# Performance work log

Measured on AMD Instinct MI355X. Metric: run time of the kernel, lower is better.

Reference implementation:

```python
import jax, jax.numpy as jnp
import numpy as np

B, C, M, NH, F_, W = 2, 8, 8, 8, 1024, 512  # batch, channels, attention_maps, heads, features, frames
HD = F_ // NH
EXP = 4


def _conv(x, w, b):
    y = jax.lax.conv_general_dilated(x, w, (1, 1), 'SAME',
                                     dimension_numbers=('NCHW', 'OIHW', 'NCHW'))
    return y + b[None, :, None, None]


def _rope(x):
    # x: (..., seq, d); lucidrains-style interleaved rotary embedding
    d, n = x.shape[-1], x.shape[-2]
    inv = 1.0 / (10000.0 ** (jnp.arange(0, d, 2, dtype=jnp.float32) / d))
    fr = jnp.repeat(jnp.arange(n, dtype=jnp.float32)[:, None] * inv[None, :], 2, axis=-1)
    cos, sin = jnp.cos(fr), jnp.sin(fr)
    xr = jnp.stack((-x[..., 1::2], x[..., 0::2]), axis=-1).reshape(x.shape)
    return x * cos + xr * sin


def _mcln(x, w, b, eps=1e-5):
    # MultichannelLayerNorm: normalize over features axis (axis=2 of B,C,F,W)
    mu = jnp.mean(x, axis=2, keepdims=True)
    var = jnp.var(x, axis=2, keepdims=True)
    return (x - mu) / jnp.sqrt(var + eps) * w[None, :, :, None] + b[None, :, :, None]


def _mclin(x, w_pw):
    # MultichannelLinear positionwise: per-channel matmul over features
    return jnp.einsum('bcfw,cgf->bcgw', x, w_pw)


def setup_inputs() -> dict:
    key = jax.random.key(0)
    ks = jax.random.split(key, 24)
    s = 0.02
    d = {
        'x': jax.random.normal(ks[0], (B, C, F_, W), jnp.float32),
        'prev_qk': jax.random.normal(ks[1], (B, M, NH, W, W), jnp.float32),
        'qconv_w': jax.random.normal(ks[2], (M, C, 3, 3), jnp.float32) * s,
        'qconv_b': jnp.zeros((M,), jnp.float32),
        'q_pw': jax.random.normal(ks[3], (M, F_, F_), jnp.float32) * s,
        'kconv_w': jax.random.normal(ks[4], (M, C, 3, 3), jnp.float32) * s,
        'kconv_b': jnp.zeros((M,), jnp.float32),
        'k_pw': jax.random.normal(ks[5], (M, F_, F_), jnp.float32) * s,
        'vconv_w': jax.random.normal(ks[6], (M, C, 3, 3), jnp.float32) * s,
        'vconv_b': jnp.zeros((M,), jnp.float32),
        'v_pw': jax.random.normal(ks[7], (M, F_, F_), jnp.float32) * s,
        'o_pw': jax.random.normal(ks[8], (M, F_, F_), jnp.float32) * s,
        'o_dw': jax.random.normal(ks[9], (M, M), jnp.float32) * s,
        'oproj_w': jax.random.normal(ks[10], (C, C + M, 3, 3), jnp.float32) * s,
        'oproj_b': jnp.zeros((C,), jnp.float32),
        'n1_w': jnp.ones((C, F_), jnp.float32),
        'n1_b': jnp.zeros((C, F_), jnp.float32),
        'c1_w': jax.random.normal(ks[11], (C * EXP, C, 3, 3), jnp.float32) * s,
        'c1_b': jnp.zeros((C * EXP,), jnp.float32),
        'c2_w': jax.random.normal(ks[12], (C, C * EXP, 3, 3), jnp.float32) * s,
        'c2_b': jnp.zeros((C,), jnp.float32),
        'n2_w': jnp.ones((C, F_), jnp.float32),
        'n2_b': jnp.zeros((C, F_), jnp.float32),
    }
    return d


def _encoder(x, prev_qk, qconv_w, qconv_b, q_pw, kconv_w, kconv_b, k_pw,
             vconv_w, vconv_b, v_pw, o_pw, o_dw, oproj_w, oproj_b,
             n1_w, n1_b, c1_w, c1_b, c2_w, c2_b, n2_w, n2_b):
    b, c, h, w = x.shape

    def heads(y):  # (B,M,F,W) -> (B,M,NH,W,HD)
        return y.transpose(0, 1, 3, 2).reshape(b, M, w, NH, HD).transpose(0, 1, 3, 2, 4)

    q = _rope(heads(_mclin(_conv(x, qconv_w, qconv_b), q_pw)))
    k = _rope(heads(_mclin(_conv(x, kconv_w, kconv_b), k_pw)))
    v = heads(_mclin(_conv(x, vconv_w, vconv_b), v_pw))

    qk = jnp.einsum('bmnqd,bmnkd->bmnqk', q, k) / jnp.sqrt(jnp.float32(h))
    qk = qk + prev_qk
    a = jnp.einsum('bmnqk,bmnkd->bmnqd', jax.nn.softmax(qk, axis=-1), v)
    a = a.transpose(0, 1, 3, 2, 4).reshape(b, M, w, NH * HD).transpose(0, 1, 3, 2)  # (B,M,F,W)
    a = jnp.einsum('bcfw,dc->bdfw', _mclin(a, o_pw), o_dw)  # depthwise o_linear
    z = _conv(jnp.concatenate((x, a), axis=1), oproj_w, oproj_b)

    hid = _mcln(x + z, n1_w, n1_b)  # dropout is identity in eval
    z2 = _conv(jax.nn.gelu(_conv(hid, c1_w, c1_b), approximate=False), c2_w, c2_b)
    out = _mcln(hid + z2, n2_w, n2_b)
    return out, qk


def reference(x, prev_qk, qconv_w, qconv_b, q_pw, kconv_w, kconv_b, k_pw,
              vconv_w, vconv_b, v_pw, o_pw, o_dw, oproj_w, oproj_b,
              n1_w, n1_b, c1_w, c1_b, c2_w, c2_b, n2_w, n2_b):
    out, qk = _encoder(x, prev_qk, qconv_w, qconv_b, q_pw, kconv_w, kconv_b, k_pw,
                       vconv_w, vconv_b, v_pw, o_pw, o_dw, oproj_w, oproj_b,
                       n1_w, n1_b, c1_w, c1_b, c2_w, c2_b, n2_w, n2_b)
    return (out, out, qk)
```

## Files before the change

### kernel.cpp

```cpp
#include <hip/hip_runtime.h>
#include <math.h>

#define B_ 2
#define C_ 8
#define M_ 8
#define NH_ 8
#define F_ 1024
#define W_ 512
#define HD_ 128
#define FW 524288L
#define PF_ 1026
#define PW_ 514

typedef __bf16 bf16_t;
typedef __bf16 bf16x8 __attribute__((ext_vector_type(8)));
typedef __bf16 bf16x4 __attribute__((ext_vector_type(4)));
typedef float f32x4 __attribute__((ext_vector_type(4)));

__device__ __forceinline__ void gload16(const void* g, void* l) {
    __builtin_amdgcn_global_load_lds(
        (const __attribute__((address_space(1))) unsigned int*)g,
        (__attribute__((address_space(3))) unsigned int*)l,
        16, 0, 0);
}

__device__ __forceinline__ float gelu_f(float v) {
    return 0.5f * v * (1.0f + erff(v * 0.70710678118f));
}

__global__ __launch_bounds__(256)
void pad_stage_k(const float* __restrict__ x, bf16_t* __restrict__ px)
{
    long i = (long)blockIdx.x * 256 + threadIdx.x;
    if (i >= (long)B_ * PF_ * PW_) return;
    int wc = (int)(i % PW_);
    long t = i / PW_;
    int fr = (int)(t % PF_);
    int b  = (int)(t / PF_);
    bf16x8 v = {};
    if (fr >= 1 && fr <= F_ && wc >= 1 && wc <= W_) {
        const float* s = x + (long)b * 8 * FW + (long)(fr - 1) * W_ + (wc - 1);
        #pragma unroll
        for (int c = 0; c < 8; ++c) v[c] = (bf16_t)s[c * FW];
    }
    *(bf16x8*)&px[i * 8] = v;
}

__global__ __launch_bounds__(256)
void borderz8_k(bf16_t* __restrict__ p8a, bf16_t* __restrict__ p8b)
{
    int i = blockIdx.x * 256 + threadIdx.x;
    if (i >= 2 * 3076) return;
    int b = i / 3076, p = i % 3076;
    int fr, wc;
    if (p < 514)       { fr = 0;    wc = p; }
    else if (p < 1028) { fr = 1025; wc = p - 514; }
    else if (p < 2052) { fr = 1 + (p - 1028); wc = 0; }
    else               { fr = 1 + (p - 2052); wc = 513; }
    long pix = ((long)b * PF_ + fr) * PW_ + wc;
    bf16x8 z = {};
    *(bf16x8*)&p8a[pix * 8] = z;
    *(bf16x8*)&p8b[pix * 8] = z;
}

__global__ __launch_bounds__(256)
void borderz32_k(bf16_t* __restrict__ p32)
{
    int i = blockIdx.x * 256 + threadIdx.x;
    if (i >= 2 * 3076) return;
    int b = i / 3076, p = i % 3076;
    int fr, wc;
    if (p < 514)       { fr = 0;    wc = p; }
    else if (p < 1028) { fr = 1025; wc = p - 514; }
    else if (p < 2052) { fr = 1 + (p - 1028); wc = 0; }
    else               { fr = 1 + (p - 2052); wc = 513; }
    long pix = ((long)b * PF_ + fr) * PW_ + wc;
    bf16x8 z = {};
    #pragma unroll
    for (int k = 0; k < 4; ++k) *(bf16x8*)&p32[pix * 32 + k * 8] = z;
}

__global__ void aprep_k(const float* __restrict__ qw, const float* __restrict__ kw,
                        const float* __restrict__ vw, const float* __restrict__ ow,
                        const float* __restrict__ c1w, const float* __restrict__ c2w,
                        const float* __restrict__ qb, const float* __restrict__ kb,
                        const float* __restrict__ vb,
                        bf16_t* __restrict__ a_qkv, bf16_t* __restrict__ a_op,
                        bf16_t* __restrict__ a_c1, bf16_t* __restrict__ a_c2,
                        float* __restrict__ bias_qkv)
{
    int mode = blockIdx.y;
    int i = blockIdx.x * 256 + threadIdx.x;
    if (mode == 0) {
        if (i < 3072) {
            int k = i & 31, co = (i >> 5) & 31, df = i >> 10;
            int tap = k >> 3, ci = k & 7;
            float v = 0.f;
            if (tap < 3) {
                if (co < 8)       v = qw[((co * 8 + ci) * 3 + df) * 3 + tap];
                else if (co < 16) v = kw[(((co - 8) * 8 + ci) * 3 + df) * 3 + tap];
                else if (co < 24) v = vw[(((co - 16) * 8 + ci) * 3 + df) * 3 + tap];
            }
            a_qkv[i] = (bf16_t)v;
        }
        if (i < 32) bias_qkv[i] = (i < 8) ? qb[i] : (i < 16) ? kb[i - 8] : (i < 24) ? vb[i - 16] : 0.f;
    } else if (mode == 1) {
        if (i < 3072) {
            int k = i & 63, co = (i >> 6) & 15, df = i >> 10;
            int src = k >> 5, r = k & 31, tap = r >> 3, ci = src * 8 + (r & 7);
            float v = 0.f;
            if (co < 8 && tap < 3) v = ow[((co * 16 + ci) * 3 + df) * 3 + tap];
            a_op[i] = (bf16_t)v;
        }
    } else if (mode == 2) {
        if (i < 3072) {
            int k = i & 31, co = (i >> 5) & 31, df = i >> 10;
            int tap = k >> 3, ci = k & 7;
            float v = (tap < 3) ? c1w[((co * 8 + ci) * 3 + df) * 3 + tap] : 0.f;
            a_c1[i] = (bf16_t)v;
        }
    } else {
        if (i < 4608) {
            int k = i % 96, co = (i / 96) & 15, df = i / (96 * 16);
            int tap = k >> 5, ci = k & 31;
            float v = (co < 8) ? c2w[((co * 32 + ci) * 3 + df) * 3 + tap] : 0.f;
            a_c2[i] = (bf16_t)v;
        }
    }
}

template<int CIN, int KSTEPS, int MFRAGS, int DUAL, int EPI>
__global__ __launch_bounds__(256)
void convg_k(const bf16_t* __restrict__ px0, const bf16_t* __restrict__ px1,
             const bf16_t* __restrict__ Ab, const float* __restrict__ bias,
             const float* __restrict__ resid, void* __restrict__ outp)
{
    const int f = blockIdx.y, b = blockIdx.z;
    const int tid = threadIdx.x, lane = tid & 63, wid = tid >> 6;
    const int l15 = lane & 15, l4 = lane >> 4;
    const int wbase = blockIdx.x * 256 + wid * 64;
    const int KW = KSTEPS * 32, M16 = MFRAGS * 16;

    bf16x8 af[3][MFRAGS][KSTEPS];
    #pragma unroll
    for (int df = 0; df < 3; ++df)
        #pragma unroll
        for (int mf = 0; mf < MFRAGS; ++mf)
            #pragma unroll
            for (int kk = 0; kk < KSTEPS; ++kk)
                af[df][mf][kk] = *(const bf16x8*)&Ab[(long)(df * M16 + mf * 16 + l15) * KW + kk * 32 + l4 * 8];

    f32x4 acc[MFRAGS][4];
    #pragma unroll
    for (int mf = 0; mf < MFRAGS; ++mf)
        #pragma unroll
        for (int nf = 0; nf < 4; ++nf)
            acc[mf][nf] = (f32x4){0.f, 0.f, 0.f, 0.f};

    #pragma unroll
    for (int df = 0; df < 3; ++df) {
        const long rowb = ((long)(b * PF_ + f + df)) * PW_ * CIN;
        #pragma unroll
        for (int nf = 0; nf < 4; ++nf) {
            const int wp = wbase + nf * 16 + l15;
            #pragma unroll
            for (int kk = 0; kk < KSTEPS; ++kk) {
                const bf16_t* src = (DUAL && kk == 1) ? px1 : px0;
                long addr = (CIN == 8) ? rowb + (long)(wp + l4) * 8
                                       : rowb + (long)(wp + kk) * 32 + l4 * 8;
                bf16x8 bv = *(const bf16x8*)&src[addr];
                #pragma unroll
                for (int mf = 0; mf < MFRAGS; ++mf)
                    acc[mf][nf] = __builtin_amdgcn_mfma_f32_16x16x32_bf16(
                        af[df][mf][kk], bv, acc[mf][nf], 0, 0, 0);
            }
        }
    }

    #pragma unroll
    for (int mf = 0; mf < MFRAGS; ++mf) {
        #pragma unroll
        for (int nf = 0; nf < 4; ++nf) {
            const int wp = wbase + nf * 16 + l15;
            if (EPI == 2) {
                const int cob = mf * 16 + l4 * 4;
                bf16x4 ov;
                #pragma unroll
                for (int r = 0; r < 4; ++r)
                    ov[r] = (bf16_t)gelu_f(acc[mf][nf][r] + bias[cob + r]);
                *(bf16x4*)&((bf16_t*)outp)[(((long)(b * PF_ + f + 1)) * PW_ + wp + 1) * 32 + cob] = ov;
            } else {
                #pragma unroll
                for (int r = 0; r < 4; ++r) {
                    const int co = mf * 16 + l4 * 4 + r;
                    float v = acc[mf][nf][r];
                    if (EPI == 0) {
                        if (co < 24)
                            ((bf16_t*)outp)[((long)(b * 24 + co)) * FW + (long)f * W_ + wp] = (bf16_t)(v + bias[co]);
                    } else {
                        if (co < 8) {
                            long oi = ((long)(b * 8 + co)) * FW + (long)f * W_ + wp;
                            ((bf16_t*)outp)[oi] = (bf16_t)(v + bias[co] + resid[oi]);
                        }
                    }
                }
            }
        }
    }
}

template<int EPI, int OUTBF>
__global__ __launch_bounds__(256)
void gemm_mfma_k(const bf16_t* __restrict__ Ab, const bf16_t* __restrict__ Bb,
                 void* __restrict__ Cb, const float* __restrict__ Addb,
                 float scale, int Kdim, int lda, int ldb, int ldc,
                 long sA, long sB, long sC_hi, long sC_lo, int zdivC,
                 long sAdd, int aMod)
{
    __shared__ bf16_t sAt[4096];
    __shared__ bf16_t sBt[4096];

    const int z = blockIdx.z;
    const bf16_t* A = Ab + (long)(z % aMod) * sA;
    const bf16_t* B = Bb + (long)z * sB;
    const int m0 = blockIdx.y * 128;
    const int n0 = blockIdx.x * 128;
    const int tid = threadIdx.x;
    const int lane = tid & 63, wid = tid >> 6;
    const int wr = (wid >> 1) * 64, wc = (wid & 1) * 64;
    const int l15 = lane & 15, l4 = lane >> 4;

    f32x4 acc[4][4];
    #pragma unroll
    for (int m = 0; m < 4; ++m)
        #pragma unroll
        for (int n = 0; n < 4; ++n)
            acc[m][n] = (f32x4){0.f, 0.f, 0.f, 0.f};

    const int srow = tid >> 2;
    const int scol = (tid & 3) * 8;
    const long gA0 = (long)(m0 + srow) * lda + scol;
    const long gA1 = (long)(m0 + 64 + srow) * lda + scol;
    const long gB0 = (long)(n0 + srow) * ldb + scol;
    const long gB1 = (long)(n0 + 64 + srow) * ldb + scol;
    bf16_t* lA = sAt + wid * 512;
    bf16_t* lB = sBt + wid * 512;

    for (int k0 = 0; k0 < Kdim; k0 += 32) {
        __syncthreads();
        gload16(A + gA0 + k0, lA);
        gload16(A + gA1 + k0, lA + 2048);
        gload16(B + gB0 + k0, lB);
        gload16(B + gB1 + k0, lB + 2048);
        __syncthreads();

        bf16x8 afr[4], bfr[4];
        #pragma unroll
        for (int m = 0; m < 4; ++m)
            afr[m] = *(const bf16x8*)&sAt[(wr + m * 16 + l15) * 32 + l4 * 8];
        #pragma unroll
        for (int n = 0; n < 4; ++n)
            bfr[n] = *(const bf16x8*)&sBt[(wc + n * 16 + l15) * 32 + l4 * 8];
        #pragma unroll
        for (int m = 0; m < 4; ++m)
            #pragma unroll
            for (int n = 0; n < 4; ++n)
                acc[m][n] = __builtin_amdgcn_mfma_f32_16x16x32_bf16(
                    afr[m], bfr[n], acc[m][n], 0, 0, 0);
    }

    if (EPI == 2) {
        #pragma unroll
        for (int m = 0; m < 4; ++m) {
            const int d0 = wr + m * 16 + l4 * 4;
            const float inv0 = __expf(-(float)(d0 >> 1) * 0.14391156507f);
            const float inv1 = __expf(-(float)((d0 >> 1) + 1) * 0.14391156507f);
            #pragma unroll
            for (int n = 0; n < 4; ++n) {
                const int col = n0 + wc + n * 16 + l15;
                float s0, c0, s1, c1;
                __sincosf((float)col * inv0, &s0, &c0);
                __sincosf((float)col * inv1, &s1, &c1);
                float v0 = acc[m][n][0], v1 = acc[m][n][1];
                float v2 = acc[m][n][2], v3 = acc[m][n][3];
                bf16x4 ov = { (bf16_t)(v0 * c0 - v1 * s0), (bf16_t)(v1 * c0 + v0 * s0),
                              (bf16_t)(v2 * c1 - v3 * s1), (bf16_t)(v3 * c1 + v2 * s1) };
                *(bf16x4*)&((bf16_t*)Cb)[(((long)z * 8 + blockIdx.y) * 512 + col) * 128 + d0] = ov;
            }
        }
        return;
    }

    const long zc = (long)(z / zdivC) * sC_hi + (long)(z % zdivC) * sC_lo;
    #pragma unroll
    for (int m = 0; m < 4; ++m) {
        #pragma unroll
        for (int n = 0; n < 4; ++n) {
            #pragma unroll
            for (int r = 0; r < 4; ++r) {
                int row = m0 + wr + m * 16 + l4 * 4 + r;
                int col = n0 + wc + n * 16 + l15;
                float v = acc[m][n][r];
                if (EPI == 1) v = v * scale + Addb[(long)z * sAdd + (long)row * ldc + col];
                long cidx = zc + (long)row * ldc + col;
                if (OUTBF) ((bf16_t*)Cb)[cidx] = (bf16_t)v;
                else       ((float*)Cb)[cidx]  = v;
            }
        }
    }
}

__global__ __launch_bounds__(256)
void tcvt_k(const bf16_t* __restrict__ in, bf16_t* __restrict__ outp, int smul, int sbase)
{
    __shared__ float tile[32][33];
    const int w0 = blockIdx.x * 32, f0 = blockIdx.y * 32;
    const int z = blockIdx.z;
    const int inSlice = (z >> 3) * smul + sbase + (z & 7);
    const long ibase = (long)inSlice * FW;
    const long obase = (long)z * FW;
    const int tx = threadIdx.x & 31, ty = threadIdx.x >> 5;
    #pragma unroll
    for (int i = 0; i < 4; ++i)
        tile[ty + i * 8][tx] = (float)in[ibase + (long)(f0 + ty + i * 8) * W_ + w0 + tx];
    __syncthreads();
    #pragma unroll
    for (int i = 0; i < 4; ++i)
        outp[obase + (long)(w0 + ty + i * 8) * F_ + f0 + tx] = (bf16_t)tile[tx][ty + i * 8];
}

__global__ __launch_bounds__(256)
void cvt_k(const float* __restrict__ in, bf16_t* __restrict__ o, int n4)
{
    int i = blockIdx.x * 256 + threadIdx.x;
    if (i < n4) {
        float4 v = ((const float4*)in)[i];
        bf16x4 r = { (bf16_t)v.x, (bf16_t)v.y, (bf16_t)v.z, (bf16_t)v.w };
        *(bf16x4*)&o[(long)i * 4] = r;
    }
}

__device__ inline float waveMax(float v) {
    #pragma unroll
    for (int o = 32; o >= 1; o >>= 1) v = fmaxf(v, __shfl_xor(v, o, 64));
    return v;
}
__device__ inline float waveSum(float v) {
    #pragma unroll
    for (int o = 32; o >= 1; o >>= 1) v += __shfl_xor(v, o, 64);
    return v;
}

__global__ __launch_bounds__(256)
void softmax_k(const float* __restrict__ S, bf16_t* __restrict__ P)
{
    const int wid = threadIdx.x >> 6, lane = threadIdx.x & 63;
    const long row = (long)blockIdx.x * 4 + wid;
    const float4* s4 = (const float4*)(S + row * 512);
    float4 a = s4[lane * 2], b = s4[lane * 2 + 1];
    float m = fmaxf(fmaxf(fmaxf(a.x, a.y), fmaxf(a.z, a.w)),
                    fmaxf(fmaxf(b.x, b.y), fmaxf(b.z, b.w)));
    m = waveMax(m);
    float e0 = __expf(a.x - m), e1 = __expf(a.y - m), e2 = __expf(a.z - m), e3 = __expf(a.w - m);
    float e4 = __expf(b.x - m), e5 = __expf(b.y - m), e6 = __expf(b.z - m), e7 = __expf(b.w - m);
    float su = waveSum(e0 + e1 + e2 + e3 + e4 + e5 + e6 + e7);
    float inv = 1.0f / su;
    bf16x8 o = { (bf16_t)(e0 * inv), (bf16_t)(e1 * inv), (bf16_t)(e2 * inv), (bf16_t)(e3 * inv),
                 (bf16_t)(e4 * inv), (bf16_t)(e5 * inv), (bf16_t)(e6 * inv), (bf16_t)(e7 * inv) };
    *(bf16x8*)(P + row * 512 + lane * 8) = o;
}

__global__ __launch_bounds__(256)
void odw_k(const bf16_t* __restrict__ t, const float* __restrict__ dw, bf16_t* __restrict__ px)
{
    long i = (long)blockIdx.x * 256 + threadIdx.x;
    int w = (int)(i & (W_ - 1));
    long q = i >> 9;
    int f = (int)(q & (F_ - 1));
    int b = (int)(q >> 10);
    const bf16_t* s = t + (long)b * 8 * FW + (long)f * W_ + w;
    float tv[8];
    #pragma unroll
    for (int c = 0; c < 8; ++c) tv[c] = (float)s[c * FW];
    bf16x8 o;
    #pragma unroll
    for (int d = 0; d < 8; ++d) {
        float a = 0.f;
        #pragma unroll
        for (int c = 0; c < 8; ++c) a += tv[c] * dw[d * 8 + c];
        o[d] = (bf16_t)a;
    }
    *(bf16x8*)&px[(((long)b * PF_ + f + 1) * PW_ + w + 1) * 8] = o;
}

template<typename TIN>
__global__ __launch_bounds__(256)
void mcln_k(const TIN* __restrict__ in, const float* __restrict__ gam,
            const float* __restrict__ bet, float* __restrict__ o1, float* __restrict__ o2,
            bf16_t* __restrict__ px)
{
    int wi = threadIdx.x & 31, fg = threadIdx.x >> 5;
    int w0 = blockIdx.x * 32;
    int c = blockIdx.y, b = blockIdx.z;
    long base = ((long)b * C_ + c) * FW + w0 + wi;
    float s = 0.f, q = 0.f;
    for (int f = fg; f < F_; f += 8) {
        float v = (float)in[base + (long)f * W_];
        s += v; q += v * v;
    }
    __shared__ float rs[8][33], rq[8][33];
    __shared__ float mu_s[32], inv_s[32];
    rs[fg][wi] = s; rq[fg][wi] = q;
    __syncthreads();
    if (fg == 0) {
        float ts = 0.f, tq = 0.f;
        for (int g = 0; g < 8; ++g) { ts += rs[g][wi]; tq += rq[g][wi]; }
        float mu = ts * (1.0f / F_);
        float var = tq * (1.0f / F_) - mu * mu;
        mu_s[wi] = mu;
        inv_s[wi] = rsqrtf(var + 1e-5f);
    }
    __syncthreads();
    float mu = mu_s[wi], inv = inv_s[wi];
    for (int f = fg; f < F_; f += 8) {
        float v = (float)in[base + (long)f * W_];
        float r = (v - mu) * inv * gam[c * F_ + f] + bet[c * F_ + f];
        long oi = base + (long)f * W_;
        o1[oi] = r;
        if (o2) o2[oi] = r;
        if (px) px[(((long)b * PF_ + f + 1) * PW_ + (w0 + wi) + 1) * 8 + c] = (bf16_t)r;
    }
}

extern "C" void kernel_launch(void* const* d_in, const int* in_sizes, int n_in,
                              void* d_out, int out_size, void* d_ws, size_t ws_size,
                              hipStream_t stream) {
    (void)in_sizes; (void)n_in; (void)out_size; (void)ws_size;
    const float* x        = (const float*)d_in[0];
    const float* prev_qk  = (const float*)d_in[1];
    const float* qconv_w  = (const float*)d_in[2];
    const float* qconv_b  = (const float*)d_in[3];
    const float* q_pw     = (const float*)d_in[4];
    const float* kconv_w  = (const float*)d_in[5];
    const float* kconv_b  = (const float*)d_in[6];
    const float* k_pw     = (const float*)d_in[7];
    const float* vconv_w  = (const float*)d_in[8];
    const float* vconv_b  = (const float*)d_in[9];
    const float* v_pw     = (const float*)d_in[10];
    const float* o_pw     = (const float*)d_in[11];
    const float* o_dw     = (const float*)d_in[12];
    const float* oproj_w  = (const float*)d_in[13];
    const float* oproj_b  = (const float*)d_in[14];
    const float* n1_w     = (const float*)d_in[15];
    const float* n1_b     = (const float*)d_in[16];
    const float* c1_w     = (const float*)d_in[17];
    const float* c1_b     = (const float*)d_in[18];
    const float* c2_w     = (const float*)d_in[19];
    const float* c2_b     = (const float*)d_in[20];
    const float* n2_w     = (const float*)d_in[21];
    const float* n2_b     = (const float*)d_in[22];

    float* out    = (float*)d_out;
    float* qk_out = out + 16777216L;

    char* wsb = (char*)d_ws;
    bf16_t* PX8  = (bf16_t*)(wsb + 0L);
    bf16_t* Wq   = (bf16_t*)(wsb + 16876032L);
    bf16_t* Wk   = (bf16_t*)(wsb + 33653248L);
    bf16_t* Wv   = (bf16_t*)(wsb + 50430464L);
    bf16_t* Wo   = (bf16_t*)(wsb + 67207680L);
    bf16_t* QR   = (bf16_t*)(wsb + 83984896L);
    bf16_t* KR   = (bf16_t*)(wsb + 100762112L);
    bf16_t* VL   = (bf16_t*)(wsb + 117539328L);
    bf16_t* QKV  = (bf16_t*)(wsb + 134316544L);
    bf16_t* XT   = (bf16_t*)(wsb + 184648192L);
    bf16_t* SH   = (bf16_t*)(wsb + 134316544L);
    bf16_t* AT   = (bf16_t*)(wsb + 201425408L);
    bf16_t* F1b  = (bf16_t*)(wsb + 83984896L);
    bf16_t* PXA2 = (bf16_t*)(wsb + 100762112L);
    bf16_t* PRE  = (bf16_t*)(wsb + 134316544L);
    float*  HID  = (float*) (wsb + 151093760L);
    bf16_t* PXH  = (bf16_t*)(wsb + 218202624L);
    bf16_t* PXC1 = (bf16_t*)(wsb + 0L);
    bf16_t* ABQ  = (bf16_t*)(wsb + 235078400L);
    bf16_t* ABO  = (bf16_t*)(wsb + 235078400L + 16384L);
    bf16_t* ABC1 = (bf16_t*)(wsb + 235078400L + 32768L);
    bf16_t* ABC2 = (bf16_t*)(wsb + 235078400L + 49152L);
    float*  BQKV = (float*) (wsb + 235078400L + 65536L);

    const dim3 cvgrid(2, F_, B_);
    const dim3 tgrid(16, 32, 16);
    const dim3 ggrid(4, 8, 16);
    const long BIG = 1 << 30;

    cvt_k<<<8192, 256, 0, stream>>>(q_pw, Wq, 2097152);
    cvt_k<<<8192, 256, 0, stream>>>(k_pw, Wk, 2097152);
    cvt_k<<<8192, 256, 0, stream>>>(v_pw, Wv, 2097152);
    cvt_k<<<8192, 256, 0, stream>>>(o_pw, Wo, 2097152);
    aprep_k<<<dim3(18, 4), 256, 0, stream>>>(qconv_w, kconv_w, vconv_w, oproj_w, c1_w, c2_w,
                                             qconv_b, kconv_b, vconv_b,
                                             ABQ, ABO, ABC1, ABC2, BQKV);
    pad_stage_k<<<4121, 256, 0, stream>>>(x, PX8);

    convg_k<8, 1, 2, 0, 0><<<cvgrid, 256, 0, stream>>>(PX8, nullptr, ABQ, BQKV, nullptr, QKV);

    tcvt_k<<<tgrid, 256, 0, stream>>>(QKV, XT, 24, 0);
    gemm_mfma_k<2, 1><<<ggrid, 256, 0, stream>>>(Wq, XT, QR, nullptr, 1.f,
        F_, F_, F_, W_, 1048576L, 524288L, 0L, 0L, 1, 0L, 8);

    tcvt_k<<<tgrid, 256, 0, stream>>>(QKV, XT, 24, 8);
    gemm_mfma_k<2, 1><<<ggrid, 256, 0, stream>>>(Wk, XT, KR, nullptr, 1.f,
        F_, F_, F_, W_, 1048576L, 524288L, 0L, 0L, 1, 0L, 8);

    tcvt_k<<<tgrid, 256, 0, stream>>>(QKV, XT, 24, 16);
    gemm_mfma_k<0, 1><<<ggrid, 256, 0, stream>>>(Wv, XT, VL, nullptr, 1.f,
        F_, F_, F_, W_, 1048576L, 524288L, 524288L, 0L, 1, 0L, 8);

    gemm_mfma_k<1, 0><<<dim3(4, 4, 128), 256, 0, stream>>>(QR, KR, qk_out, prev_qk,
        0.03125f, HD_, HD_, HD_, W_, 65536L, 65536L, 262144L, 0L, 1, 262144L, (int)BIG);
    softmax_k<<<16384, 256, 0, stream>>>(qk_out, SH);
    gemm_mfma_k<0, 1><<<dim3(1, 4, 128), 256, 0, stream>>>(SH, VL, AT, nullptr, 1.f,
        W_, W_, W_, F_, 262144L, 65536L, 524288L, 128L, 8, 0L, (int)BIG);

    gemm_mfma_k<0, 1><<<ggrid, 256, 0, stream>>>(Wo, AT, F1b, nullptr, 1.f,
        F_, F_, F_, W_, 1048576L, 524288L, 524288L, 0L, 1, 0L, 8);
    odw_k<<<4096, 256, 0, stream>>>(F1b, o_dw, PXA2);
    borderz8_k<<<25, 256, 0, stream>>>(PXA2, PXH);

    convg_k<8, 2, 1, 1, 1><<<cvgrid, 256, 0, stream>>>(PX8, PXA2, ABO, oproj_b, x, PRE);
    borderz32_k<<<25, 256, 0, stream>>>(PXC1);

    mcln_k<bf16_t><<<dim3(16, 8, 2), 256, 0, stream>>>(PRE, n1_w, n1_b, HID, nullptr, PXH);

    convg_k<8, 1, 2, 0, 2><<<cvgrid, 256, 0, stream>>>(PXH, nullptr, ABC1, c1_b, nullptr, PXC1);
    convg_k<32, 3, 1, 0, 1><<<cvgrid, 256, 0, stream>>>(PXC1, nullptr, ABC2, c2_b, HID, PRE);
    mcln_k<bf16_t><<<dim3(16, 8, 2), 256, 0, stream>>>(PRE, n2_w, n2_b, out, out + 8388608L, nullptr);
}
```

Baseline: 705.8 us.

## Fuse fp32 weight conversion into GEMM loads, widen K tile, batch transposes

```diff
diff --git a/kernel.cpp b/kernel.cpp
--- a/kernel.cpp
+++ b/kernel.cpp
@@ -209,20 +209,18 @@
     }
 }
 
-template<int EPI, int OUTBF>
-__global__ __launch_bounds__(256)
-void gemm_mfma_k(const bf16_t* __restrict__ Ab, const bf16_t* __restrict__ Bb,
+template<int EPI, int OUTBF, int AF32>
+__global__ __launch_bounds__(256)
+void gemm_mfma_k(const void* __restrict__ Ab_, const bf16_t* __restrict__ Bb,
                  void* __restrict__ Cb, const float* __restrict__ Addb,
                  float scale, int Kdim, int lda, int ldb, int ldc,
                  long sA, long sB, long sC_hi, long sC_lo, int zdivC,
                  long sAdd, int aMod)
 {
-    __shared__ bf16_t sAt[4096];
-    __shared__ bf16_t sBt[4096];
+    __shared__ bf16_t sAt[8192];
+    __shared__ bf16_t sBt[8192];
 
     const int z = blockIdx.z;
-    const bf16_t* A = Ab + (long)(z % aMod) * sA;
-    const bf16_t* B = Bb + (long)z * sB;
     const int m0 = blockIdx.y * 128;
     const int n0 = blockIdx.x * 128;
     const int tid = threadIdx.x;
@@ -230,6 +228,10 @@
     const int wr = (wid >> 1) * 64, wc = (wid & 1) * 64;
     const int l15 = lane & 15, l4 = lane >> 4;
 
+    const bf16_t* A16 = AF32 ? nullptr : (const bf16_t*)Ab_ + (long)(z % aMod) * sA;
+    const float*  A32 = AF32 ? (const float*)Ab_ + (long)(z % aMod) * sA : nullptr;
+    const bf16_t* B = Bb + (long)z * sB;
+
     f32x4 acc[4][4];
     #pragma unroll
     for (int m = 0; m < 4; ++m)
@@ -237,36 +239,61 @@
         for (int n = 0; n < 4; ++n)
             acc[m][n] = (f32x4){0.f, 0.f, 0.f, 0.f};
 
-    const int srow = tid >> 2;
-    const int scol = (tid & 3) * 8;
-    const long gA0 = (long)(m0 + srow) * lda + scol;
-    const long gA1 = (long)(m0 + 64 + srow) * lda + scol;
-    const long gB0 = (long)(n0 + srow) * ldb + scol;
-    const long gB1 = (long)(n0 + 64 + srow) * ldb + scol;
-    bf16_t* lA = sAt + wid * 512;
-    bf16_t* lB = sBt + wid * 512;
-
-    for (int k0 = 0; k0 < Kdim; k0 += 32) {
+    const int grow = wid * 8 + (lane >> 3);
+    const int gslot = lane & 7;
+    const int arow = tid >> 1;
+    const int akg  = (tid & 1) * 4;
+
+    for (int k0 = 0; k0 < Kdim; k0 += 64) {
         __syncthreads();
-        gload16(A + gA0 + k0, lA);
-        gload16(A + gA1 + k0, lA + 2048);
-        gload16(B + gB0 + k0, lB);
-        gload16(B + gB1 + k0, lB + 2048);
+        if (AF32) {
+            const float* asrc = A32 + (long)(m0 + arow) * lda + k0 + akg * 8;
+            const int swz = arow & 7;
+            #pragma unroll
+            for (int j = 0; j < 4; ++j) {
+                float4 u = ((const float4*)asrc)[j * 2];
+                float4 v = ((const float4*)asrc)[j * 2 + 1];
+                bf16x8 w8 = { (bf16_t)u.x, (bf16_t)u.y, (bf16_t)u.z, (bf16_t)u.w,
+                              (bf16_t)v.x, (bf16_t)v.y, (bf16_t)v.z, (bf16_t)v.w };
+                *(bf16x8*)&sAt[arow * 64 + (((akg + j) ^ swz) << 3)] = w8;
+            }
+        } else {
+            #pragma unroll
+            for (int r = 0; r < 4; ++r) {
+                const int row = r * 32 + grow;
+                gload16(A16 + (long)(m0 + row) * lda + k0 + ((gslot ^ (row & 7)) << 3),
+                        sAt + r * 2048 + wid * 512);
+            }
+        }
+        #pragma unroll
+        for (int r = 0; r < 4; ++r) {
+            const int row = r * 32 + grow;
+            gload16(B + (long)(n0 + row) * ldb + k0 + ((gslot ^ (row & 7)) << 3),
+                    sBt + r * 2048 + wid * 512);
+        }
         __syncthreads();
 
-        bf16x8 afr[4], bfr[4];
-        #pragma unroll
-        for (int m = 0; m < 4; ++m)
-            afr[m] = *(const bf16x8*)&sAt[(wr + m * 16 + l15) * 32 + l4 * 8];
-        #pragma unroll
-        for (int n = 0; n < 4; ++n)
-            bfr[n] = *(const bf16x8*)&sBt[(wc + n * 16 + l15) * 32 + l4 * 8];
-        #pragma unroll
-        for (int m = 0; m < 4; ++m)
-            #pragma unroll
-            for (int n = 0; n < 4; ++n)
-                acc[m][n] = __builtin_amdgcn_mfma_f32_16x16x32_bf16(
-                    afr[m], bfr[n], acc[m][n], 0, 0, 0);
+        bf16x8 afr[4][2], bfr[4][2];
+        #pragma unroll
+        for (int m = 0; m < 4; ++m) {
+            const int row = wr + m * 16 + l15, swz = row & 7;
+            afr[m][0] = *(const bf16x8*)&sAt[row * 64 + ((l4 ^ swz) << 3)];
+            afr[m][1] = *(const bf16x8*)&sAt[row * 64 + (((4 + l4) ^ swz) << 3)];
+        }
+        #pragma unroll
+        for (int n = 0; n < 4; ++n) {
+            const int row = wc + n * 16 + l15, swz = row & 7;
+            bfr[n][0] = *(const bf16x8*)&sBt[row * 64 + ((l4 ^ swz) << 3)];
+            bfr[n][1] = *(const bf16x8*)&sBt[row * 64 + (((4 + l4) ^ swz) << 3)];
+        }
+        #pragma unroll
+        for (int kk = 0; kk < 2; ++kk)
+            #pragma unroll
+            for (int m = 0; m < 4; ++m)
+                #pragma unroll
+                for (int n = 0; n < 4; ++n)
+                    acc[m][n] = __builtin_amdgcn_mfma_f32_16x16x32_bf16(
+                        afr[m][kk], bfr[n][kk], acc[m][n], 0, 0, 0);
     }
 
     if (EPI == 2) {
@@ -311,12 +338,13 @@
 }
 
 __global__ __launch_bounds__(256)
-void tcvt_k(const bf16_t* __restrict__ in, bf16_t* __restrict__ outp, int smul, int sbase)
+void tcvt_k(const bf16_t* __restrict__ in, bf16_t* __restrict__ outp)
 {
     __shared__ float tile[32][33];
     const int w0 = blockIdx.x * 32, f0 = blockIdx.y * 32;
     const int z = blockIdx.z;
-    const int inSlice = (z >> 3) * smul + sbase + (z & 7);
+    const int path = z >> 4, bm = z & 15;
+    const int inSlice = (bm >> 3) * 24 + path * 8 + (bm & 7);
     const long ibase = (long)inSlice * FW;
     const long obase = (long)z * FW;
     const int tx = threadIdx.x & 31, ty = threadIdx.x >> 5;
@@ -327,17 +355,6 @@
     #pragma unroll
     for (int i = 0; i < 4; ++i)
         outp[obase + (long)(w0 + ty + i * 8) * F_ + f0 + tx] = (bf16_t)tile[tx][ty + i * 8];
-}
-
-__global__ __launch_bounds__(256)
-void cvt_k(const float* __restrict__ in, bf16_t* __restrict__ o, int n4)
-{
-    int i = blockIdx.x * 256 + threadIdx.x;
-    if (i < n4) {
-        float4 v = ((const float4*)in)[i];
-        bf16x4 r = { (bf16_t)v.x, (bf16_t)v.y, (bf16_t)v.z, (bf16_t)v.w };
-        *(bf16x4*)&o[(long)i * 4] = r;
-    }
 }
 
 __device__ inline float waveMax(float v) {
@@ -465,38 +482,30 @@
 
     char* wsb = (char*)d_ws;
     bf16_t* PX8  = (bf16_t*)(wsb + 0L);
-    bf16_t* Wq   = (bf16_t*)(wsb + 16876032L);
-    bf16_t* Wk   = (bf16_t*)(wsb + 33653248L);
-    bf16_t* Wv   = (bf16_t*)(wsb + 50430464L);
-    bf16_t* Wo   = (bf16_t*)(wsb + 67207680L);
-    bf16_t* QR   = (bf16_t*)(wsb + 83984896L);
-    bf16_t* KR   = (bf16_t*)(wsb + 100762112L);
-    bf16_t* VL   = (bf16_t*)(wsb + 117539328L);
-    bf16_t* QKV  = (bf16_t*)(wsb + 134316544L);
-    bf16_t* XT   = (bf16_t*)(wsb + 184648192L);
-    bf16_t* SH   = (bf16_t*)(wsb + 134316544L);
-    bf16_t* AT   = (bf16_t*)(wsb + 201425408L);
-    bf16_t* F1b  = (bf16_t*)(wsb + 83984896L);
-    bf16_t* PXA2 = (bf16_t*)(wsb + 100762112L);
-    bf16_t* PRE  = (bf16_t*)(wsb + 134316544L);
-    float*  HID  = (float*) (wsb + 151093760L);
-    bf16_t* PXH  = (bf16_t*)(wsb + 218202624L);
-    bf16_t* PXC1 = (bf16_t*)(wsb + 0L);
-    bf16_t* ABQ  = (bf16_t*)(wsb + 235078400L);
-    bf16_t* ABO  = (bf16_t*)(wsb + 235078400L + 16384L);
-    bf16_t* ABC1 = (bf16_t*)(wsb + 235078400L + 32768L);
-    bf16_t* ABC2 = (bf16_t*)(wsb + 235078400L + 49152L);
-    float*  BQKV = (float*) (wsb + 235078400L + 65536L);
+    bf16_t* XT48 = (bf16_t*)(wsb + 16876032L);
+    bf16_t* QR   = (bf16_t*)(wsb + 67207680L);
+    bf16_t* KR   = (bf16_t*)(wsb + 83984896L);
+    bf16_t* VL   = (bf16_t*)(wsb + 100762112L);
+    bf16_t* QKV  = (bf16_t*)(wsb + 117539328L);
+    bf16_t* SH   = (bf16_t*)(wsb + 16876032L);
+    bf16_t* AT   = (bf16_t*)(wsb + 117539328L);
+    bf16_t* F1b  = (bf16_t*)(wsb + 134316544L);
+    bf16_t* PXA2 = (bf16_t*)(wsb + 83984896L);
+    float*  HID  = (float*) (wsb + 16876032L);
+    bf16_t* PXC1 = (bf16_t*)(wsb + 50430464L);
+    bf16_t* PRE  = (bf16_t*)(wsb + 151093760L);
+    bf16_t* PXH  = (bf16_t*)(wsb + 167870976L);
+    bf16_t* ABQ  = (bf16_t*)(wsb + 184748032L);
+    bf16_t* ABO  = (bf16_t*)(wsb + 184748032L + 16384L);
+    bf16_t* ABC1 = (bf16_t*)(wsb + 184748032L + 32768L);
+    bf16_t* ABC2 = (bf16_t*)(wsb + 184748032L + 49152L);
+    float*  BQKV = (float*) (wsb + 184748032L + 65536L);
 
     const dim3 cvgrid(2, F_, B_);
-    const dim3 tgrid(16, 32, 16);
+    const dim3 tgrid(16, 32, 48);
     const dim3 ggrid(4, 8, 16);
     const long BIG = 1 << 30;
 
-    cvt_k<<<8192, 256, 0, stream>>>(q_pw, Wq, 2097152);
-    cvt_k<<<8192, 256, 0, stream>>>(k_pw, Wk, 2097152);
-    cvt_k<<<8192, 256, 0, stream>>>(v_pw, Wv, 2097152);
-    cvt_k<<<8192, 256, 0, stream>>>(o_pw, Wo, 2097152);
     aprep_k<<<dim3(18, 4), 256, 0, stream>>>(qconv_w, kconv_w, vconv_w, oproj_w, c1_w, c2_w,
                                              qconv_b, kconv_b, vconv_b,
                                              ABQ, ABO, ABC1, ABC2, BQKV);
@@ -504,25 +513,21 @@
 
     convg_k<8, 1, 2, 0, 0><<<cvgrid, 256, 0, stream>>>(PX8, nullptr, ABQ, BQKV, nullptr, QKV);
 
-    tcvt_k<<<tgrid, 256, 0, stream>>>(QKV, XT, 24, 0);
-    gemm_mfma_k<2, 1><<<ggrid, 256, 0, stream>>>(Wq, XT, QR, nullptr, 1.f,
+    tcvt_k<<<tgrid, 256, 0, stream>>>(QKV, XT48);
+    gemm_mfma_k<2, 1, 1><<<ggrid, 256, 0, stream>>>(q_pw, XT48, QR, nullptr, 1.f,
         F_, F_, F_, W_, 1048576L, 524288L, 0L, 0L, 1, 0L, 8);
-
-    tcvt_k<<<tgrid, 256, 0, stream>>>(QKV, XT, 24, 8);
-    gemm_mfma_k<2, 1><<<ggrid, 256, 0, stream>>>(Wk, XT, KR, nullptr, 1.f,
+    gemm_mfma_k<2, 1, 1><<<ggrid, 256, 0, stream>>>(k_pw, XT48 + 16L * FW, KR, nullptr, 1.f,
         F_, F_, F_, W_, 1048576L, 524288L, 0L, 0L, 1, 0L, 8);
-
-    tcvt_k<<<tgrid, 256, 0, stream>>>(QKV, XT, 24, 16);
-    gemm_mfma_k<0, 1><<<ggrid, 256, 0, stream>>>(Wv, XT, VL, nullptr, 1.f,
+    gemm_mfma_k<0, 1, 1><<<ggrid, 256, 0, stream>>>(v_pw, XT48 + 32L * FW, VL, nullptr, 1.f,
         F_, F_, F_, W_, 1048576L, 524288L, 524288L, 0L, 1, 0L, 8);
 
-    gemm_mfma_k<1, 0><<<dim3(4, 4, 128), 256, 0, stream>>>(QR, KR, qk_out, prev_qk,
+    gemm_mfma_k<1, 0, 0><<<dim3(4, 4, 128), 256, 0, stream>>>(QR, KR, qk_out, prev_qk,
         0.03125f, HD_, HD_, HD_, W_, 65536L, 65536L, 262144L, 0L, 1, 262144L, (int)BIG);
     softmax_k<<<16384, 256, 0, stream>>>(qk_out, SH);
-    gemm_mfma_k<0, 1><<<dim3(1, 4, 128), 256, 0, stream>>>(SH, VL, AT, nullptr, 1.f,
+    gemm_mfma_k<0, 1, 0><<<dim3(1, 4, 128), 256, 0, stream>>>(SH, VL, AT, nullptr, 1.f,
         W_, W_, W_, F_, 262144L, 65536L, 524288L, 128L, 8, 0L, (int)BIG);
 
-    gemm_mfma_k<0, 1><<<ggrid, 256, 0, stream>>>(Wo, AT, F1b, nullptr, 1.f,
+    gemm_mfma_k<0, 1, 1><<<ggrid, 256, 0, stream>>>(o_pw, AT, F1b, nullptr, 1.f,
         F_, F_, F_, W_, 1048576L, 524288L, 524288L, 0L, 1, 0L, 8);
     odw_k<<<4096, 256, 0, stream>>>(F1b, o_dw, PXA2);
     borderz8_k<<<25, 256, 0, stream>>>(PXA2, PXH);
```

After: 706.1 us. About the same (+0.0%).
